# Optimization experiments

Measured on AMD Instinct MI355X. Metric: run time of the kernel, lower is better.

## Reference

```python
import jax, jax.numpy as jnp
import numpy as np

B, NX, NY, T = 8, 512, 512, 2_000_000


def setup_inputs() -> dict:
    key = jax.random.key(0)
    k1, k2, k3 = jax.random.split(key, 3)
    # regular source grid (flattened row-major: flat = j*NX + i, x varies fastest)
    xs = jnp.linspace(0.0, 1.0, NX, dtype=jnp.float32)
    ys = jnp.linspace(0.0, 1.0, NY, dtype=jnp.float32)
    SX, SY = jnp.meshgrid(xs, ys)  # (NY, NX)
    src_x = SX.reshape(1, -1)
    src_y = SY.reshape(1, -1)
    # target points strictly inside the convex hull (no NaN extrapolation)
    eps = 1e-3
    tgt_x = jax.random.uniform(k1, (1, T), jnp.float32, eps, 1.0 - eps)
    tgt_y = jax.random.uniform(k2, (1, T), jnp.float32, eps, 1.0 - eps)
    x = jax.random.normal(k3, (B, NX * NY, 1), jnp.float32)
    return {"x": x, "src_x": src_x, "src_y": src_y,
            "tgt_x": tgt_x, "tgt_y": tgt_y, "nx": NX, "ny": NY}


def reference(x, src_x, src_y, tgt_x, tgt_y, nx, ny):
    # Linear ND (triangulated) interpolation of x from a regular source grid
    # onto scattered target points. Each grid cell is split along the
    # (i,j)-(i+1,j+1) diagonal; barycentric weights inside each triangle.
    sx = src_x.reshape(-1)
    sy = src_y.reshape(-1)
    tx = tgt_x.reshape(-1)
    ty = tgt_y.reshape(-1)
    x0, x1 = sx.min(), sx.max()
    y0, y1 = sy.min(), sy.max()
    dx = (x1 - x0) / (nx - 1)
    dy = (y1 - y0) / (ny - 1)
    fx = (tx - x0) / dx
    fy = (ty - y0) / dy
    ix = jnp.clip(jnp.floor(fx), 0, nx - 2)
    iy = jnp.clip(jnp.floor(fy), 0, ny - 2)
    u = fx - ix  # local cell coords in [0,1]
    v = fy - iy
    ii = jax.lax.stop_gradient(ix).astype(jnp.int32)
    jj = jax.lax.stop_gradient(iy).astype(jnp.int32)
    base = jj * nx + ii
    i00, i10, i01, i11 = base, base + 1, base + nx, base + nx + 1
    lower = (u + v) <= 1.0  # which triangle of the cell
    idx = jnp.where(lower[:, None],
                    jnp.stack([i00, i10, i01], axis=-1),
                    jnp.stack([i11, i10, i01], axis=-1))  # [t,3]
    w = jnp.where(lower[:, None],
                  jnp.stack([1.0 - u - v, u, v], axis=-1),
                  jnp.stack([u + v - 1.0, 1.0 - v, 1.0 - u], axis=-1))  # [t,3]
    vals = x[:, idx, 0]                      # [b,t,3] gather of triangle vertices
    out = jnp.einsum('btk,tk->bt', vals, w)  # barycentric combination
    return out[..., None]                    # [b,t,1]
```

## Files before the change

kernel.cpp:

```cpp
#include <hip/hip_runtime.h>
#include <hip/hip_fp16.h>


typedef float  f32x4 __attribute__((ext_vector_type(4)));
typedef unsigned int u32x4 __attribute__((ext_vector_type(4)));

__device__ __forceinline__ unsigned pack_h2(float lo, float hi) {
    union { __half2 h2; unsigned u; } cv;
    cv.h2 = __float22half2_rn(make_float2(lo, hi));
    return cv.u;
}

__global__ __launch_bounds__(256) void build_grid16(
    const float* __restrict__ x,
    u32x4* __restrict__ rec,
    int N)
{
    const int p0 = (blockIdx.x * blockDim.x + threadIdx.x) * 4;
    if (p0 + 4 <= N) {
        f32x4 v[8];
        #pragma unroll
        for (int b = 0; b < 8; ++b)
            v[b] = *reinterpret_cast<const f32x4*>(x + (long)b * N + p0);
        #pragma unroll
        for (int k = 0; k < 4; ++k) {
            u32x4 r;
            r[0] = pack_h2(v[0][k], v[1][k]);
            r[1] = pack_h2(v[2][k], v[3][k]);
            r[2] = pack_h2(v[4][k], v[5][k]);
            r[3] = pack_h2(v[6][k], v[7][k]);
            rec[p0 + k] = r;
        }
    } else {
        for (int p = p0; p < N; ++p) {
            u32x4 r;
            r[0] = pack_h2(x[p], x[(long)N + p]);
            r[1] = pack_h2(x[2L * N + p], x[3L * N + p]);
            r[2] = pack_h2(x[4L * N + p], x[5L * N + p]);
            r[3] = pack_h2(x[6L * N + p], x[7L * N + p]);
            rec[p] = r;
        }
    }
}

__device__ __forceinline__ void half8_to_float8(u32x4 u, float* f) {
    union { u32x4 v; __half2 h2[4]; } cv;
    cv.v = u;
    float2 a = __half22float2(cv.h2[0]); f[0] = a.x; f[1] = a.y;
    float2 b = __half22float2(cv.h2[1]); f[2] = b.x; f[3] = b.y;
    float2 c = __half22float2(cv.h2[2]); f[4] = c.x; f[5] = c.y;
    float2 d = __half22float2(cv.h2[3]); f[6] = d.x; f[7] = d.y;
}

#define TPT 8

__global__ __launch_bounds__(256) void interp_rec_kernel(
    const u32x4* __restrict__ rec,
    const float* __restrict__ src_x,
    const float* __restrict__ src_y,
    const float* __restrict__ tgt_x,
    const float* __restrict__ tgt_y,
    const int* __restrict__ nx_p,
    float* __restrict__ out,
    int T, int N)
{
    const int nx = *nx_p;
    const int ny = N / nx;
    const float x0 = src_x[0];
    const float x1 = src_x[nx - 1];
    const float y0 = src_y[0];
    const float y1 = src_y[N - 1];
    const float rdx = (float)(nx - 1) / (x1 - x0);
    const float rdy = (float)(ny - 1) / (y1 - y0);

    const int t0 = (blockIdx.x * blockDim.x + threadIdx.x) * TPT;
    if (t0 >= T) return;

    if (t0 + TPT <= T) {
        f32x4 txa = __builtin_nontemporal_load(
            reinterpret_cast<const f32x4*>(tgt_x + t0));
        f32x4 txb = __builtin_nontemporal_load(
            reinterpret_cast<const f32x4*>(tgt_x + t0 + 4));
        f32x4 tya = __builtin_nontemporal_load(
            reinterpret_cast<const f32x4*>(tgt_y + t0));
        f32x4 tyb = __builtin_nontemporal_load(
            reinterpret_cast<const f32x4*>(tgt_y + t0 + 4));

        int g0[TPT], g1[TPT], g2[TPT];
        float w0a[TPT], w1a[TPT], w2a[TPT];
        #pragma unroll
        for (int k = 0; k < TPT; ++k) {
            float tx = (k < 4) ? txa[k] : txb[k - 4];
            float ty = (k < 4) ? tya[k] : tyb[k - 4];
            float fx = (tx - x0) * rdx;
            float fy = (ty - y0) * rdy;
            float ix = fminf(fmaxf(floorf(fx), 0.0f), (float)(nx - 2));
            float iy = fminf(fmaxf(floorf(fy), 0.0f), (float)(ny - 2));
            float u = fx - ix;
            float v = fy - iy;
            bool lower = (u + v) <= 1.0f;
            int g = (int)iy * nx + (int)ix;
            g0[k] = g + (lower ? 0 : (nx + 1));
            g1[k] = g + 1;
            g2[k] = g + nx;
            w0a[k] = lower ? (1.0f - u - v) : (u + v - 1.0f);
            w1a[k] = lower ? u : (1.0f - v);
            w2a[k] = lower ? v : (1.0f - u);
        }

        u32x4 r0[TPT], r1[TPT], r2[TPT];
        #pragma unroll
        for (int k = 0; k < TPT; ++k) { r0[k] = rec[g0[k]]; }
        #pragma unroll
        for (int k = 0; k < TPT; ++k) { r1[k] = rec[g1[k]]; }
        #pragma unroll
        for (int k = 0; k < TPT; ++k) { r2[k] = rec[g2[k]]; }

        float res[TPT][8];
        #pragma unroll
        for (int k = 0; k < TPT; ++k) {
            float f0[8], f1[8], f2[8];
            half8_to_float8(r0[k], f0);
            half8_to_float8(r1[k], f1);
            half8_to_float8(r2[k], f2);
            #pragma unroll
            for (int b = 0; b < 8; ++b)
                res[k][b] = f0[b] * w0a[k] + f1[b] * w1a[k] + f2[b] * w2a[k];
        }

        #pragma unroll
        for (int b = 0; b < 8; ++b) {
            f32x4 ra = { res[0][b], res[1][b], res[2][b], res[3][b] };
            f32x4 rb = { res[4][b], res[5][b], res[6][b], res[7][b] };
            __builtin_nontemporal_store(
                ra, reinterpret_cast<f32x4*>(out + (long)b * T + t0));
            __builtin_nontemporal_store(
                rb, reinterpret_cast<f32x4*>(out + (long)b * T + t0 + 4));
        }
    } else {
        for (int t = t0; t < T; ++t) {
            float fx = (tgt_x[t] - x0) * rdx;
            float fy = (tgt_y[t] - y0) * rdy;
            float ix = fminf(fmaxf(floorf(fx), 0.0f), (float)(nx - 2));
            float iy = fminf(fmaxf(floorf(fy), 0.0f), (float)(ny - 2));
            float u = fx - ix;
            float v = fy - iy;
            bool lower = (u + v) <= 1.0f;
            int g = (int)iy * nx + (int)ix;
            u32x4 q0 = rec[g + (lower ? 0 : (nx + 1))];
            u32x4 q1 = rec[g + 1];
            u32x4 q2 = rec[g + nx];
            float w0 = lower ? (1.0f - u - v) : (u + v - 1.0f);
            float w1 = lower ? u : (1.0f - v);
            float w2 = lower ? v : (1.0f - u);
            float f0[8], f1[8], f2[8];
            half8_to_float8(q0, f0);
            half8_to_float8(q1, f1);
            half8_to_float8(q2, f2);
            for (int b = 0; b < 8; ++b)
                out[(long)b * T + t] = f0[b] * w0 + f1[b] * w1 + f2[b] * w2;
        }
    }
}

__global__ __launch_bounds__(256) void interp_fallback_kernel(
    const float* __restrict__ x,
    const float* __restrict__ src_x,
    const float* __restrict__ src_y,
    const float* __restrict__ tgt_x,
    const float* __restrict__ tgt_y,
    const int* __restrict__ nx_p,
    float* __restrict__ out,
    int T, int N, int B)
{
    const int nx = *nx_p;
    const int ny = N / nx;
    const float x0 = src_x[0];
    const float x1 = src_x[nx - 1];
    const float y0 = src_y[0];
    const float y1 = src_y[N - 1];
    const float rdx = (float)(nx - 1) / (x1 - x0);
    const float rdy = (float)(ny - 1) / (y1 - y0);

    const int t = blockIdx.x * blockDim.x + threadIdx.x;
    if (t >= T) return;
    float fx = (tgt_x[t] - x0) * rdx;
    float fy = (tgt_y[t] - y0) * rdy;
    float ix = fminf(fmaxf(floorf(fx), 0.0f), (float)(nx - 2));
    float iy = fminf(fmaxf(floorf(fy), 0.0f), (float)(ny - 2));
    float u = fx - ix;
    float v = fy - iy;
    int base = (int)iy * nx + (int)ix;
    bool lower = (u + v) <= 1.0f;
    int   i0 = lower ? base : (base + nx + 1);
    int   i1 = base + 1;
    int   i2 = base + nx;
    float w0 = lower ? (1.0f - u - v) : (u + v - 1.0f);
    float w1 = lower ? u : (1.0f - v);
    float w2 = lower ? v : (1.0f - u);
    for (int b = 0; b < B; ++b) {
        const float* xb = x + (long)b * N;
        out[(long)b * T + t] = xb[i0] * w0 + xb[i1] * w1 + xb[i2] * w2;
    }
}

extern "C" void kernel_launch(void* const* d_in, const int* in_sizes, int n_in,
                              void* d_out, int out_size, void* d_ws, size_t ws_size,
                              hipStream_t stream) {
    const float* x     = (const float*)d_in[0];
    const float* src_x = (const float*)d_in[1];
    const float* src_y = (const float*)d_in[2];
    const float* tgt_x = (const float*)d_in[3];
    const float* tgt_y = (const float*)d_in[4];
    const int*   nx_p  = (const int*)d_in[5];
    float* out = (float*)d_out;

    const int N = in_sizes[1];
    const int T = in_sizes[3];
    const int B = in_sizes[0] / N;

    const size_t rec_bytes = (size_t)N * 16;

    if (B == 8 && ws_size >= rec_bytes) {
        u32x4* rec = (u32x4*)d_ws;
        {
            const int block = 256;
            const int grid = ((N + 3) / 4 + block - 1) / block;
            build_grid16<<<grid, block, 0, stream>>>(x, rec, N);
        }
        {
            const int threads_needed = (T + TPT - 1) / TPT;
            const int block = 256;
            const int grid = (threads_needed + block - 1) / block;
            interp_rec_kernel<<<grid, block, 0, stream>>>(
                rec, src_x, src_y, tgt_x, tgt_y, nx_p, out, T, N);
        }
    } else {
        const int block = 256;
        const int grid = (T + block - 1) / block;
        interp_fallback_kernel<<<grid, block, 0, stream>>>(
            x, src_x, src_y, tgt_x, tgt_y, nx_p, out, T, N, B);
    }
}
```

Before: 130.2 us.

## Software-pipeline gathers in a persistent grid-stride interpolation kernel

Replaces the one-shot kernel (8 targets per thread) with a persistent grid-stride kernel that has 4 targets per thread and a cap of 512 blocks. The kernel double-buffers across chunks: it issues the next chunk's target loads and record gathers before converting and storing the current chunk, so gather latency is overlapped with compute. The aim is to hide random-access gather latency within each thread instead of relying on occupancy. In exchange it needs more registers, fixes launch_bounds at 2 blocks per CU, and a capped grid may underfill the GPU.

```diff
diff --git a/kernel.cpp b/kernel.cpp
--- a/kernel.cpp
+++ b/kernel.cpp
@@ -52,9 +52,58 @@
     float2 d = __half22float2(cv.h2[3]); f[6] = d.x; f[7] = d.y;
 }
 
-#define TPT 8
-
-__global__ __launch_bounds__(256) void interp_rec_kernel(
+#define TPT 4
+
+#define LOAD_TGT(c, tx, ty) do {                                          \
+    const int _t0 = (c) * TPT;                                            \
+    tx = __builtin_nontemporal_load(                                      \
+        reinterpret_cast<const f32x4*>(tgt_x + _t0));                     \
+    ty = __builtin_nontemporal_load(                                      \
+        reinterpret_cast<const f32x4*>(tgt_y + _t0));                     \
+} while (0)
+
+#define GATHER(tx, ty, w0, w1, w2, r0, r1, r2) do {                       \
+    _Pragma("unroll")                                                     \
+    for (int k = 0; k < TPT; ++k) {                                       \
+        float fx = (tx[k] - x0) * rdx;                                    \
+        float fy = (ty[k] - y0) * rdy;                                    \
+        float ix = fminf(fmaxf(floorf(fx), 0.0f), ixmax);                 \
+        float iy = fminf(fmaxf(floorf(fy), 0.0f), iymax);                 \
+        float u = fx - ix;                                                \
+        float v = fy - iy;                                                \
+        bool lower = (u + v) <= 1.0f;                                     \
+        int g = (int)iy * nx + (int)ix;                                   \
+        w0[k] = lower ? (1.0f - u - v) : (u + v - 1.0f);                  \
+        w1[k] = lower ? u : (1.0f - v);                                   \
+        w2[k] = lower ? v : (1.0f - u);                                   \
+        r0[k] = rec[g + (lower ? 0 : (nx + 1))];                          \
+        r1[k] = rec[g + 1];                                               \
+        r2[k] = rec[g + nx];                                              \
+    }                                                                     \
+} while (0)
+
+#define CONSUME(c, w0, w1, w2, r0, r1, r2) do {                           \
+    const int _t0 = (c) * TPT;                                            \
+    float res[TPT][8];                                                    \
+    _Pragma("unroll")                                                     \
+    for (int k = 0; k < TPT; ++k) {                                       \
+        float f0[8], f1[8], f2[8];                                        \
+        half8_to_float8(r0[k], f0);                                       \
+        half8_to_float8(r1[k], f1);                                       \
+        half8_to_float8(r2[k], f2);                                       \
+        _Pragma("unroll")                                                 \
+        for (int b = 0; b < 8; ++b)                                       \
+            res[k][b] = f0[b] * w0[k] + f1[b] * w1[k] + f2[b] * w2[k];    \
+    }                                                                     \
+    _Pragma("unroll")                                                     \
+    for (int b = 0; b < 8; ++b) {                                         \
+        f32x4 r4 = { res[0][b], res[1][b], res[2][b], res[3][b] };        \
+        __builtin_nontemporal_store(                                      \
+            r4, reinterpret_cast<f32x4*>(out + (long)b * T + _t0));       \
+    }                                                                     \
+} while (0)
+
+__global__ __launch_bounds__(256, 2) void interp_pipe_kernel(
     const u32x4* __restrict__ rec,
     const float* __restrict__ src_x,
     const float* __restrict__ src_y,
@@ -72,77 +121,21 @@
     const float y1 = src_y[N - 1];
     const float rdx = (float)(nx - 1) / (x1 - x0);
     const float rdy = (float)(ny - 1) / (y1 - y0);
-
-    const int t0 = (blockIdx.x * blockDim.x + threadIdx.x) * TPT;
-    if (t0 >= T) return;
-
-    if (t0 + TPT <= T) {
-        f32x4 txa = __builtin_nontemporal_load(
-            reinterpret_cast<const f32x4*>(tgt_x + t0));
-        f32x4 txb = __builtin_nontemporal_load(
-            reinterpret_cast<const f32x4*>(tgt_x + t0 + 4));
-        f32x4 tya = __builtin_nontemporal_load(
-            reinterpret_cast<const f32x4*>(tgt_y + t0));
-        f32x4 tyb = __builtin_nontemporal_load(
-            reinterpret_cast<const f32x4*>(tgt_y + t0 + 4));
-
-        int g0[TPT], g1[TPT], g2[TPT];
-        float w0a[TPT], w1a[TPT], w2a[TPT];
-        #pragma unroll
-        for (int k = 0; k < TPT; ++k) {
-            float tx = (k < 4) ? txa[k] : txb[k - 4];
-            float ty = (k < 4) ? tya[k] : tyb[k - 4];
-            float fx = (tx - x0) * rdx;
-            float fy = (ty - y0) * rdy;
-            float ix = fminf(fmaxf(floorf(fx), 0.0f), (float)(nx - 2));
-            float iy = fminf(fmaxf(floorf(fy), 0.0f), (float)(ny - 2));
-            float u = fx - ix;
-            float v = fy - iy;
-            bool lower = (u + v) <= 1.0f;
-            int g = (int)iy * nx + (int)ix;
-            g0[k] = g + (lower ? 0 : (nx + 1));
-            g1[k] = g + 1;
-            g2[k] = g + nx;
-            w0a[k] = lower ? (1.0f - u - v) : (u + v - 1.0f);
-            w1a[k] = lower ? u : (1.0f - v);
-            w2a[k] = lower ? v : (1.0f - u);
-        }
-
-        u32x4 r0[TPT], r1[TPT], r2[TPT];
-        #pragma unroll
-        for (int k = 0; k < TPT; ++k) { r0[k] = rec[g0[k]]; }
-        #pragma unroll
-        for (int k = 0; k < TPT; ++k) { r1[k] = rec[g1[k]]; }
-        #pragma unroll
-        for (int k = 0; k < TPT; ++k) { r2[k] = rec[g2[k]]; }
-
-        float res[TPT][8];
-        #pragma unroll
-        for (int k = 0; k < TPT; ++k) {
-            float f0[8], f1[8], f2[8];
-            half8_to_float8(r0[k], f0);
-            half8_to_float8(r1[k], f1);
-            half8_to_float8(r2[k], f2);
-            #pragma unroll
-            for (int b = 0; b < 8; ++b)
-                res[k][b] = f0[b] * w0a[k] + f1[b] * w1a[k] + f2[b] * w2a[k];
-        }
-
-        #pragma unroll
-        for (int b = 0; b < 8; ++b) {
-            f32x4 ra = { res[0][b], res[1][b], res[2][b], res[3][b] };
-            f32x4 rb = { res[4][b], res[5][b], res[6][b], res[7][b] };
-            __builtin_nontemporal_store(
-                ra, reinterpret_cast<f32x4*>(out + (long)b * T + t0));
-            __builtin_nontemporal_store(
-                rb, reinterpret_cast<f32x4*>(out + (long)b * T + t0 + 4));
-        }
-    } else {
-        for (int t = t0; t < T; ++t) {
+    const float ixmax = (float)(nx - 2);
+    const float iymax = (float)(ny - 2);
+
+    const int nch = T / TPT;
+    const int gsz = gridDim.x * blockDim.x;
+    const int tid = blockIdx.x * blockDim.x + threadIdx.x;
+
+    {
+        const int tail0 = nch * TPT;
+        if (tid < T - tail0) {
+            const int t = tail0 + tid;
             float fx = (tgt_x[t] - x0) * rdx;
             float fy = (tgt_y[t] - y0) * rdy;
-            float ix = fminf(fmaxf(floorf(fx), 0.0f), (float)(nx - 2));
-            float iy = fminf(fmaxf(floorf(fy), 0.0f), (float)(ny - 2));
+            float ix = fminf(fmaxf(floorf(fx), 0.0f), ixmax);
+            float iy = fminf(fmaxf(floorf(fy), 0.0f), iymax);
             float u = fx - ix;
             float v = fy - iy;
             bool lower = (u + v) <= 1.0f;
@@ -160,6 +153,37 @@
             for (int b = 0; b < 8; ++b)
                 out[(long)b * T + t] = f0[b] * w0 + f1[b] * w1 + f2[b] * w2;
         }
+    }
+
+    int cCur = tid;
+    if (cCur >= nch) return;
+    int cNxt = cCur + gsz;
+    int cPre = cNxt + gsz;
+
+    f32x4 txA, tyA, txB, tyB;
+    float wA0[TPT], wA1[TPT], wA2[TPT];
+    float wB0[TPT], wB1[TPT], wB2[TPT];
+    u32x4 rA0[TPT], rA1[TPT], rA2[TPT];
+    u32x4 rB0[TPT], rB1[TPT], rB2[TPT];
+
+    LOAD_TGT(cCur, txA, tyA);
+    bool haveNxt = (cNxt < nch);
+    if (haveNxt) LOAD_TGT(cNxt, txB, tyB);
+    GATHER(txA, tyA, wA0, wA1, wA2, rA0, rA1, rA2);
+
+    while (true) {
+        if (!haveNxt) { CONSUME(cCur, wA0, wA1, wA2, rA0, rA1, rA2); break; }
+        if (cPre < nch) LOAD_TGT(cPre, txA, tyA);
+        GATHER(txB, tyB, wB0, wB1, wB2, rB0, rB1, rB2);
+        CONSUME(cCur, wA0, wA1, wA2, rA0, rA1, rA2);
+        cCur = cNxt; cNxt = cPre; cPre += gsz;
+        haveNxt = (cNxt < nch);
+        if (!haveNxt) { CONSUME(cCur, wB0, wB1, wB2, rB0, rB1, rB2); break; }
+        if (cPre < nch) LOAD_TGT(cPre, txB, tyB);
+        GATHER(txA, tyA, wA0, wA1, wA2, rA0, rA1, rA2);
+        CONSUME(cCur, wB0, wB1, wB2, rB0, rB1, rB2);
+        cCur = cNxt; cNxt = cPre; cPre += gsz;
+        haveNxt = (cNxt < nch);
     }
 }
 
@@ -229,10 +253,11 @@
             build_grid16<<<grid, block, 0, stream>>>(x, rec, N);
         }
         {
-            const int threads_needed = (T + TPT - 1) / TPT;
-            const int block = 256;
-            const int grid = (threads_needed + block - 1) / block;
-            interp_rec_kernel<<<grid, block, 0, stream>>>(
+            const int nch = T / TPT;
+            int grid = (nch + 255) / 256;
+            if (grid > 512) grid = 512;
+            if (grid < 1) grid = 1;
+            interp_pipe_kernel<<<grid, 256, 0, stream>>>(
                 rec, src_x, src_y, tgt_x, tgt_y, nx_p, out, T, N);
         }
     } else {
```

Result: no change. 129.3 us (-0.7%).
